# Performance work log

Measured on AMD Instinct MI355X. Metric: run time of the kernel, lower is better.

The kernel has to match this reference:

```python
import jax, jax.numpy as jnp
import numpy as np

TAU = 2.0
V_TH = 1.0
V_RST = 0.0
BN_EPS = 1e-5

# --- ATan surrogate-gradient Heaviside spike (spikingjelly default, alpha=2) ---
@jax.custom_vjp
def atan_spike(x):
    return (x >= 0.0).astype(x.dtype)

def _atan_fwd(x):
    return atan_spike(x), x

def _atan_bwd(x, g):
    alpha = 2.0
    return (g * (alpha / 2.0) / (1.0 + (jnp.pi / 2.0 * alpha * x) ** 2),)

atan_spike.defvjp(_atan_fwd, _atan_bwd)

# --- multi-step LIF (decay_input=False, hard reset, detach_reset=True) ---
def lif(x_seq):
    def step(v, xt):
        v = v - (v - V_RST) / TAU + xt            # charge
        s = atan_spike(v - V_TH)                  # fire
        sd = jax.lax.stop_gradient(s)             # detach_reset
        v = (1.0 - sd) * v + sd * V_RST           # hard reset
        return v, s
    v0 = jnp.full(x_seq.shape[1:], V_RST, x_seq.dtype)
    _, spikes = jax.lax.scan(step, v0, x_seq)
    return spikes

def setup_inputs() -> dict:
    key = jax.random.key(0)
    k1, k2 = jax.random.split(key)
    T, B, N = 64, 256, 512
    x = jax.random.normal(k1, (T, B, N), dtype=jnp.float32)
    # xavier-uniform-like init for Linear weight [out, in]
    bound = float(np.sqrt(6.0 / (N + N)))
    W = jax.random.uniform(k2, (N, N), minval=-bound, maxval=bound, dtype=jnp.float32)
    gamma = jnp.ones((N,), jnp.float32)
    beta = jnp.zeros((N,), jnp.float32)
    return {"x": x, "W": W, "gamma": gamma, "beta": beta}

def reference(x, W, gamma, beta):
    # x: [T, B, N]
    T, B, N = x.shape
    # spatial / temporal spiking gates (reduction='mean')
    spatial = lif(x.mean(axis=-1, keepdims=True))   # [T, B, 1]
    temporal = lif(x.mean(axis=0, keepdims=True))   # [1, B, N] (scan over length-1 T)
    s = (x * spatial) * (x * temporal)
    x = x + s
    x = lif(x)
    # Linear (no bias): y = x @ W.T
    x = jnp.einsum('tbn,mn->tbm', x, W)
    # BatchNorm1d over channels N, stats over flattened T*B (training mode)
    xf = x.reshape(T * B, N)
    mu = xf.mean(axis=0)
    var = xf.var(axis=0)
    xf = (xf - mu) * jax.lax.rsqrt(var + BN_EPS) * gamma + beta
    x = xf.reshape(T, B, N)
    x = lif(x)
    return x
```

## Files before the change

kernel.cpp:

```cpp
#include <hip/hip_runtime.h>
#include <hip/hip_bf16.h>
#include <math.h>

#define TT 64
#define BB 256
#define NN 512

typedef __attribute__((ext_vector_type(8)))  short s16x8;
typedef __attribute__((ext_vector_type(16))) float f32x16;

__device__ __forceinline__ void gload16(const void* g, void* l) {
  __builtin_amdgcn_global_load_lds(
      (const __attribute__((address_space(1))) unsigned int*)g,
      (__attribute__((address_space(3))) unsigned int*)l, 16, 0, 0);
}


__global__ __launch_bounds__(256) void wprep_kernel(
    const float* __restrict__ W, unsigned short* __restrict__ WT) {
  int i = blockIdx.x * 256 + threadIdx.x;
  int m = i >> 9, k = i & 511;
  float v = W[i];
  unsigned u0 = __float_as_uint(v);
  unsigned h0 = (u0 + 0x7FFFu + ((u0 >> 16) & 1u)) >> 16;
  float f0 = __uint_as_float(h0 << 16);
  float r1 = v - f0;
  unsigned u1 = __float_as_uint(r1);
  unsigned h1 = (u1 + 0x7FFFu + ((u1 >> 16) & 1u)) >> 16;
  float f1 = __uint_as_float(h1 << 16);
  float r2 = r1 - f1;
  unsigned u2 = __float_as_uint(r2);
  unsigned h2 = (u2 + 0x7FFFu + ((u2 >> 16) & 1u)) >> 16;
  int cg = m >> 5, kc = k >> 4;
  size_t base = ((size_t)(cg * 3) * 32 + kc) * 512
              + ((m & 31) + 32 * ((k >> 3) & 1)) * 8 + (k & 7);
  WT[base        ] = (unsigned short)h0;
  WT[base + 16384] = (unsigned short)h1;
  WT[base + 32768] = (unsigned short)h2;
}

__global__ __launch_bounds__(512) void frontend_kernel(
    const float* __restrict__ x, unsigned short* __restrict__ spkT) {
  extern __shared__ float xs[];
  __shared__ float rms[TT];
  __shared__ float sp[TT];
  int b = blockIdx.x, tid = threadIdx.x;
  int l = tid & 63, w = tid >> 6;
  #pragma unroll
  for (int p = 0; p < 16; ++p) {
    int f = p * 512 + tid;
    int t = f >> 7, c4 = f & 127;
    gload16(x + (size_t)t * (BB * NN) + (size_t)b * NN + c4 * 4,
            (char*)xs + p * 8192 + w * 1024);
  }
  __syncthreads();
  #pragma unroll
  for (int j = 0; j < 8; ++j) {
    int t = w * 8 + j;
    float s = 0.f;
    #pragma unroll
    for (int q = 0; q < 8; ++q) s += xs[t * 512 + q * 64 + l];
    #pragma unroll
    for (int off = 32; off; off >>= 1) s += __shfl_xor(s, off);
    if (l == 0) rms[t] = s;
  }
  float cs = 0.f;
  for (int t = 0; t < TT; ++t) cs += xs[t * 512 + tid];
  __syncthreads();
  if (w == 0) {
    float myrm = rms[l];
    float v = 0.f;
    unsigned long long mask = 0ull;
    #pragma unroll
    for (int t = 0; t < TT; ++t) {
      float m = __shfl(myrm, t) * (1.0f / 512.0f);
      v = v * 0.5f + m;
      if (v >= 1.0f) { mask |= (1ull << t); v = 0.f; }
    }
    sp[l] = (float)((mask >> l) & 1ull);
  }
  __syncthreads();
  float te = (cs * (1.0f / 64.0f) >= 1.0f) ? 1.0f : 0.0f;
  float v = 0.f;
  unsigned short* sb = spkT + (size_t)(b >> 5) * 16384 + (tid >> 4) * 512
                     + (b & 31) * 8 + ((tid >> 3) & 1) * 256 + (tid & 7);
  for (int t = 0; t < TT; ++t) {
    float xv = xs[t * 512 + tid];
    float a = xv + (xv * sp[t]) * (xv * te);
    v = v * 0.5f + a;
    unsigned short s = (v >= 1.0f) ? 0x3F80 : 0;
    sb[(size_t)t * 131072] = s;
    if (s) v = 0.f;
  }
}

__global__ __launch_bounds__(256) void gemm_kernel(
    const unsigned short* __restrict__ AT, const unsigned short* __restrict__ WT,
    float* __restrict__ C, float* __restrict__ pS, float* __restrict__ pQ) {
  __shared__ unsigned char sm[3][16384];
  int tid = threadIdx.x;
  int l = tid & 63, w = tid >> 6;
  int wr = w >> 1, wc = w & 1;
  int bx = blockIdx.x, by = blockIdx.y;
  int row0 = bx * 128, col0 = by * 128;
  int lr = l & 31, lh = l >> 5;

  f32x16 acc[2][2];
  #pragma unroll
  for (int f = 0; f < 2; ++f)
    #pragma unroll
    for (int g = 0; g < 2; ++g)
      #pragma unroll
      for (int j = 0; j < 16; ++j) acc[f][g][j] = 0.f;

  auto STAGE = [&](unsigned char* lbase, int ks) {
    if (w == 0) {
      #pragma unroll
      for (int j = 0; j < 4; ++j)
        gload16((const char*)AT + ((size_t)(bx * 4 + j) * 32 + ks) * 1024 + l * 16,
                lbase + j * 1024);
    } else {
      int comp = w - 1;
      #pragma unroll
      for (int cg = 0; cg < 4; ++cg)
        gload16((const char*)WT + (((size_t)(by * 4 + cg) * 3 + comp) * 32 + ks) * 1024 + l * 16,
                lbase + 4096 + (cg * 3 + comp) * 1024);
    }
  };

  STAGE(sm[0], 0);
  STAGE(sm[1], 1);
  for (int ks = 0; ks < 32; ++ks) {
    asm volatile("s_waitcnt lgkmcnt(0)" ::: "memory");
    if (ks < 31) asm volatile("s_waitcnt vmcnt(4)" ::: "memory");
    else         asm volatile("s_waitcnt vmcnt(0)" ::: "memory");
    asm volatile("s_barrier" ::: "memory");
    if (ks < 30) STAGE(sm[(ks + 2) % 3], ks + 2);
    const unsigned char* bp = sm[ks % 3];
    s16x8 a[2], bf[2][3];
    #pragma unroll
    for (int f = 0; f < 2; ++f)
      a[f] = *(const s16x8*)(bp + (wr * 2 + f) * 1024 + l * 16);
    #pragma unroll
    for (int g = 0; g < 2; ++g)
      #pragma unroll
      for (int c = 0; c < 3; ++c)
        bf[g][c] = *(const s16x8*)(bp + 4096 + ((wc * 2 + g) * 3 + c) * 1024 + l * 16);
    __builtin_amdgcn_s_setprio(1);
    #pragma unroll
    for (int c = 0; c < 3; ++c)
      #pragma unroll
      for (int f = 0; f < 2; ++f)
        #pragma unroll
        for (int g = 0; g < 2; ++g)
          acc[f][g] = __builtin_amdgcn_mfma_f32_32x32x16_bf16(a[f], bf[g][c], acc[f][g], 0, 0, 0);
    __builtin_amdgcn_s_setprio(0);
  }

  #pragma unroll
  for (int g = 0; g < 2; ++g) {
    int col = col0 + wc * 64 + g * 32 + lr;
    float sy = 0.f, sq = 0.f;
    #pragma unroll
    for (int f = 0; f < 2; ++f)
      #pragma unroll
      for (int j = 0; j < 16; ++j) {
        float y = acc[f][g][j];
        int row = row0 + wr * 64 + f * 32 + (j & 3) + 8 * (j >> 2) + 4 * lh;
        C[(size_t)row * NN + col] = y;
        sy += y; sq += y * y;
      }
    sy += __shfl_xor(sy, 32);
    sq += __shfl_xor(sq, 32);
    if (lh == 0) {
      pS[(size_t)col * 256 + bx * 2 + wr] = sy;
      pQ[(size_t)col * 256 + bx * 2 + wr] = sq;
    }
  }
}

__global__ __launch_bounds__(512) void bnstatsB_kernel(
    const float* __restrict__ pS, const float* __restrict__ pQ,
    float* __restrict__ mu, float* __restrict__ inv) {
  int tid = threadIdx.x;
  int ch = blockIdx.x * 64 + (tid >> 3), p = tid & 7;
  const float* ps = pS + (size_t)ch * 256 + p * 32;
  const float* pq = pQ + (size_t)ch * 256 + p * 32;
  float s = 0.f, q = 0.f;
  #pragma unroll
  for (int i = 0; i < 32; ++i) { s += ps[i]; q += pq[i]; }
  #pragma unroll
  for (int off = 1; off < 8; off <<= 1) { s += __shfl_xor(s, off); q += __shfl_xor(q, off); }
  if (p == 0) {
    float mean = s * (1.0f / 16384.0f);
    float var  = q * (1.0f / 16384.0f) - mean * mean;
    mu[ch] = mean;
    inv[ch] = 1.0f / sqrtf(var + 1e-5f);
  }
}

__global__ __launch_bounds__(256) void final_kernel(
    float* __restrict__ y, const float* __restrict__ mu, const float* __restrict__ inv,
    const float* __restrict__ gamma, const float* __restrict__ beta) {
  int g = blockIdx.x * 256 + threadIdx.x;
  int b = g >> 9, m = g & 511;
  float MU = mu[m], IV = inv[m], G = gamma[m], BE = beta[m];
  float* p = y + (size_t)b * NN + m;
  const size_t st = (size_t)BB * NN;
  float buf[16], nxt[16];
  #pragma unroll
  for (int j = 0; j < 16; ++j) buf[j] = p[(size_t)j * st];
  float v = 0.f;
  #pragma unroll
  for (int t0 = 0; t0 < 64; t0 += 16) {
    if (t0 + 16 < 64) {
      #pragma unroll
      for (int j = 0; j < 16; ++j) nxt[j] = p[(size_t)(t0 + 16 + j) * st];
    }
    #pragma unroll
    for (int j = 0; j < 16; ++j) {
      float xb = (buf[j] - MU) * IV * G + BE;
      v = v * 0.5f + xb;
      float s = (v >= 1.0f) ? 1.0f : 0.0f;
      p[(size_t)(t0 + j) * st] = s;
      if (s != 0.f) v = 0.f;
    }
    #pragma unroll
    for (int j = 0; j < 16; ++j) buf[j] = nxt[j];
  }
}

extern "C" void kernel_launch(void* const* d_in, const int* in_sizes, int n_in,
                              void* d_out, int out_size, void* d_ws, size_t ws_size,
                              hipStream_t stream) {
  const float* x     = (const float*)d_in[0];
  const float* W     = (const float*)d_in[1];
  const float* gamma = (const float*)d_in[2];
  const float* beta  = (const float*)d_in[3];
  float* out = (float*)d_out;

  char* ws = (char*)d_ws;
  unsigned short* WT   = (unsigned short*)ws;
  unsigned short* spkT = (unsigned short*)(ws + 1572864);
  float* pS    = (float*)(ws + 18350080);
  float* pQ    = (float*)(ws + 18874368);
  float* bn_mu = (float*)(ws + 19398656);
  float* bn_inv= (float*)(ws + 19400704);

  wprep_kernel<<<dim3(1024), dim3(256), 0, stream>>>(W, WT);
  frontend_kernel<<<dim3(BB), dim3(512), 131072, stream>>>(x, spkT);
  gemm_kernel<<<dim3(128, 4), dim3(256), 0, stream>>>(spkT, WT, out, pS, pQ);
  bnstatsB_kernel<<<dim3(8), dim3(512), 0, stream>>>(pS, pQ, bn_mu, bn_inv);
  final_kernel<<<dim3(512), dim3(256), 0, stream>>>(out, bn_mu, bn_inv, gamma, beta);
}
```

Baseline: 146.0 us.

## Double-buffer GEMM with 32-wide K tiles and component-major weight layout

The GEMM pipeline moves from a 3-stage ring of 16-wide K tiles to a 2-stage double buffer of 32-wide K tiles, halving the number of barriers and loop iterations. Global-to-LDS loads are now spread evenly across all four waves instead of one wave loading A and three loading the weight components. The weight prep layout changes to component-major so each bf16 split component is contiguous. The cost is a full vmcnt(0) wait each iteration, which reduces prefetch depth and may expose more load latency.

```diff
diff --git a/kernel.cpp b/kernel.cpp
--- a/kernel.cpp
+++ b/kernel.cpp
@@ -32,11 +32,11 @@
   unsigned u2 = __float_as_uint(r2);
   unsigned h2 = (u2 + 0x7FFFu + ((u2 >> 16) & 1u)) >> 16;
   int cg = m >> 5, kc = k >> 4;
-  size_t base = ((size_t)(cg * 3) * 32 + kc) * 512
+  size_t base = ((size_t)cg * 32 + kc) * 512
               + ((m & 31) + 32 * ((k >> 3) & 1)) * 8 + (k & 7);
-  WT[base        ] = (unsigned short)h0;
-  WT[base + 16384] = (unsigned short)h1;
-  WT[base + 32768] = (unsigned short)h2;
+  WT[base         ] = (unsigned short)h0;
+  WT[base + 262144] = (unsigned short)h1;
+  WT[base + 524288] = (unsigned short)h2;
 }
 
 __global__ __launch_bounds__(512) void frontend_kernel(
@@ -97,7 +97,7 @@
 __global__ __launch_bounds__(256) void gemm_kernel(
     const unsigned short* __restrict__ AT, const unsigned short* __restrict__ WT,
     float* __restrict__ C, float* __restrict__ pS, float* __restrict__ pQ) {
-  __shared__ unsigned char sm[3][16384];
+  __shared__ unsigned char sm[2][32768];
   int tid = threadIdx.x;
   int l = tid & 63, w = tid >> 6;
   int wr = w >> 1, wc = w & 1;
@@ -113,48 +113,52 @@
       #pragma unroll
       for (int j = 0; j < 16; ++j) acc[f][g][j] = 0.f;
 
-  auto STAGE = [&](unsigned char* lbase, int ks) {
-    if (w == 0) {
-      #pragma unroll
-      for (int j = 0; j < 4; ++j)
-        gload16((const char*)AT + ((size_t)(bx * 4 + j) * 32 + ks) * 1024 + l * 16,
-                lbase + j * 1024);
-    } else {
-      int comp = w - 1;
-      #pragma unroll
-      for (int cg = 0; cg < 4; ++cg)
-        gload16((const char*)WT + (((size_t)(by * 4 + cg) * 3 + comp) * 32 + ks) * 1024 + l * 16,
-                lbase + 4096 + (cg * 3 + comp) * 1024);
+  auto STAGE = [&](unsigned char* lbase, int kt) {
+    #pragma unroll
+    for (int j = 0; j < 2; ++j) {
+      int c = j * 4 + w;
+      int rg = bx * 4 + (c >> 1), kc = kt * 2 + (c & 1);
+      gload16((const char*)AT + ((size_t)rg * 32 + kc) * 1024 + l * 16,
+              lbase + c * 1024);
+    }
+    #pragma unroll
+    for (int j = 0; j < 6; ++j) {
+      int c = j * 4 + w;
+      int comp = c >> 3, cg = (c >> 1) & 3, kc = kt * 2 + (c & 1);
+      gload16((const char*)WT + (((size_t)comp * 16 + by * 4 + cg) * 32 + kc) * 1024 + l * 16,
+              lbase + 8192 + c * 1024);
     }
   };
 
   STAGE(sm[0], 0);
-  STAGE(sm[1], 1);
-  for (int ks = 0; ks < 32; ++ks) {
+  #pragma unroll
+  for (int kt = 0; kt < 16; ++kt) {
     asm volatile("s_waitcnt lgkmcnt(0)" ::: "memory");
-    if (ks < 31) asm volatile("s_waitcnt vmcnt(4)" ::: "memory");
-    else         asm volatile("s_waitcnt vmcnt(0)" ::: "memory");
+    asm volatile("s_waitcnt vmcnt(0)" ::: "memory");
     asm volatile("s_barrier" ::: "memory");
-    if (ks < 30) STAGE(sm[(ks + 2) % 3], ks + 2);
-    const unsigned char* bp = sm[ks % 3];
-    s16x8 a[2], bf[2][3];
-    #pragma unroll
-    for (int f = 0; f < 2; ++f)
-      a[f] = *(const s16x8*)(bp + (wr * 2 + f) * 1024 + l * 16);
-    #pragma unroll
-    for (int g = 0; g < 2; ++g)
+    if (kt < 15) STAGE(sm[(kt + 1) & 1], kt + 1);
+    const unsigned char* bp = sm[kt & 1];
+    #pragma unroll
+    for (int kc2 = 0; kc2 < 2; ++kc2) {
+      s16x8 a[2], bf[2][3];
+      #pragma unroll
+      for (int f = 0; f < 2; ++f)
+        a[f] = *(const s16x8*)(bp + ((wr * 2 + f) * 2 + kc2) * 1024 + l * 16);
+      #pragma unroll
+      for (int g = 0; g < 2; ++g)
+        #pragma unroll
+        for (int c = 0; c < 3; ++c)
+          bf[g][c] = *(const s16x8*)(bp + 8192 + ((c * 4 + wc * 2 + g) * 2 + kc2) * 1024 + l * 16);
+      __builtin_amdgcn_s_setprio(1);
       #pragma unroll
       for (int c = 0; c < 3; ++c)
-        bf[g][c] = *(const s16x8*)(bp + 4096 + ((wc * 2 + g) * 3 + c) * 1024 + l * 16);
-    __builtin_amdgcn_s_setprio(1);
-    #pragma unroll
-    for (int c = 0; c < 3; ++c)
-      #pragma unroll
-      for (int f = 0; f < 2; ++f)
         #pragma unroll
-        for (int g = 0; g < 2; ++g)
-          acc[f][g] = __builtin_amdgcn_mfma_f32_32x32x16_bf16(a[f], bf[g][c], acc[f][g], 0, 0, 0);
-    __builtin_amdgcn_s_setprio(0);
+        for (int f = 0; f < 2; ++f)
+          #pragma unroll
+          for (int g = 0; g < 2; ++g)
+            acc[f][g] = __builtin_amdgcn_mfma_f32_32x32x16_bf16(a[f], bf[g][c], acc[f][g], 0, 0, 0);
+      __builtin_amdgcn_s_setprio(0);
+    }
   }
 
   #pragma unroll
```

After: 145.7 us. Within noise of the previous version (-0.2%).
